# Optimization experiments

Measured on AMD Instinct MI355X. Metric: run time of the kernel, lower is better.

Reference implementation:

```python
import jax, jax.numpy as jnp
import numpy as np

BN_EPS = 1e-5
DIST_EPS = 1e-8


def setup_inputs() -> dict:
    key = jax.random.key(0)
    ks = jax.random.split(key, 10)
    B, Ni, Mi = 4, 16384, 4096
    C1, C2 = 64, 64
    Cin = C1 + C2  # 128, mlp=[128,128,128]
    inp = {
        "unknown": jax.random.normal(ks[0], (B * Ni, 3), dtype=jnp.float32),
        "unknown_batch_cnt": np.full(B, Ni, dtype=np.int64),
        "known": jax.random.normal(ks[1], (B * Mi, 3), dtype=jnp.float32),
        "known_batch_cnt": np.full(B, Mi, dtype=np.int64),
        "unknown_feats": jax.random.normal(ks[2], (B * Ni, C1), dtype=jnp.float32),
        "known_feats": jax.random.normal(ks[3], (B * Mi, C2), dtype=jnp.float32),
        "W1": jax.random.normal(ks[4], (128, Cin), dtype=jnp.float32) * 0.05,
        "g1": jnp.ones((128,), dtype=jnp.float32),
        "b1": jnp.zeros((128,), dtype=jnp.float32),
        "W2": jax.random.normal(ks[5], (128, 128), dtype=jnp.float32) * 0.05,
        "g2": jnp.ones((128,), dtype=jnp.float32),
        "b2": jnp.zeros((128,), dtype=jnp.float32),
    }
    return inp


def _three_nn(u, k):
    # u: (B,Ni,3), k: (B,Mi,3) -> dist (B,Ni,3), idx (B,Ni,3) within each batch
    d2 = (jnp.sum(u * u, -1)[:, :, None] + jnp.sum(k * k, -1)[:, None, :]
          - 2.0 * jnp.einsum("bnd,bmd->bnm", u, k))  # (B,Ni,Mi)
    neg_d2, idx = jax.lax.top_k(-d2, 3)
    dist = jnp.sqrt(jnp.maximum(-neg_d2, 0.0))
    return dist, idx


def _bn_relu(y, g, b):
    # BatchNorm2d over the point dim (training-mode batch stats), then ReLU
    mu = jnp.mean(y, axis=0)
    var = jnp.mean((y - mu) ** 2, axis=0)
    return jax.nn.relu((y - mu) * jax.lax.rsqrt(var + BN_EPS) * g + b)


def reference(unknown, unknown_batch_cnt, known, known_batch_cnt,
              unknown_feats, known_feats, W1, g1, b1, W2, g2, b2):
    ucnt = np.asarray(unknown_batch_cnt)
    kcnt = np.asarray(known_batch_cnt)
    B = ucnt.shape[0]
    Ni, Mi = int(ucnt[0]), int(kcnt[0])  # equal-count ragged batches
    C2 = known_feats.shape[1]

    u = unknown.reshape(B, Ni, 3)
    k = known.reshape(B, Mi, 3)
    dist, idx = _three_nn(u, k)

    dist_recip = 1.0 / (dist + DIST_EPS)
    weight = dist_recip / jnp.sum(dist_recip, axis=-1, keepdims=True)  # (B,Ni,3)

    kf = known_feats.reshape(B, Mi, C2)
    gathered = kf[jnp.arange(B)[:, None, None], idx]  # (B,Ni,3,C2)
    interp = jnp.sum(weight[..., None] * gathered, axis=2).reshape(B * Ni, C2)

    x = jnp.concatenate([interp, unknown_feats], axis=1)  # (N, C2+C1)
    x = _bn_relu(x @ W1.T, g1, b1)
    x = _bn_relu(x @ W2.T, g2, b2)
    return x
```

## Files before the change

### kernel.cpp

```cpp
#include <hip/hip_runtime.h>
#include <hip/hip_bf16.h>

#define GRID  32
#define NCELL (GRID * GRID * GRID)
#define H     0.3125f
#define INVH  3.2f
#define OFF   5.0f
#define SUBW  8
#define XPAD  136
#define NREP  16

using f32x4  = __attribute__((ext_vector_type(4))) float;
using bf16x8 = __attribute__((ext_vector_type(8))) short;

static __device__ inline short f2bs(float f) {
  __hip_bfloat16 h = __float2bfloat16(f);
  return __builtin_bit_cast(short, h);
}
static __device__ inline float bs2f(short s) {
  return __bfloat162float(__builtin_bit_cast(__hip_bfloat16, s));
}
static __device__ inline int cellco(float x) {
  int c = (int)((x + OFF) * INVH);
  return min(GRID - 1, max(0, c));
}

#define INS3(B0, B1, B2, J0, J1, J2, dv, mv)           \
  {                                                    \
    bool q0 = dv < B0, q1 = dv < B1, q2 = dv < B2;     \
    float P0 = B0, P1 = B1; int Q0 = J0, Q1 = J1;      \
    B2 = q1 ? P1 : (q2 ? dv : B2);                     \
    J2 = q1 ? Q1 : (q2 ? mv : J2);                     \
    B1 = q0 ? P0 : (q1 ? dv : P1);                     \
    J1 = q0 ? Q0 : (q1 ? mv : Q1);                     \
    B0 = q0 ? dv : P0;                                 \
    J0 = q0 ? mv : Q0;                                 \
  }
#define INSF(dv, mv) INS3(b0, b1, b2, j0, j1, j2, dv, mv)

#define MERGE3(lo_mk, hi_mk)                                                        \
  for (int mk = lo_mk; mk <= hi_mk; mk <<= 1) {                                     \
    float ob0 = __shfl_xor(b0, mk), ob1 = __shfl_xor(b1, mk), ob2 = __shfl_xor(b2, mk); \
    int   oj0 = __shfl_xor(j0, mk), oj1 = __shfl_xor(j1, mk), oj2 = __shfl_xor(j2, mk); \
    INSF(ob0, oj0); INSF(ob1, oj1); INSF(ob2, oj2);                                 \
  }

__global__ __launch_bounds__(256) void zero_k(int4* __restrict__ dst, int n4) {
  int i = blockIdx.x * 256 + threadIdx.x;
  if (i < n4) dst[i] = int4{0, 0, 0, 0};
}

__global__ __launch_bounds__(256) void hist_k(
    const float* __restrict__ known, int Mtot, int Mi,
    const float* __restrict__ unknown, int Ntot,
    int* __restrict__ khist, int* __restrict__ qhist,
    int* __restrict__ kcell, int* __restrict__ qcell,
    const float* __restrict__ W1, const float* __restrict__ W2,
    __hip_bfloat16* __restrict__ Wb1, __hip_bfloat16* __restrict__ Wb2) {
  int i = blockIdx.x * 256 + threadIdx.x;
  if (i < 128 * 128) {
    Wb1[i] = __float2bfloat16(W1[i]);
    Wb2[i] = __float2bfloat16(W2[i]);
  }
  if (i < Mtot) {
    int b = i / Mi;
    float x = known[(size_t)i * 3], y = known[(size_t)i * 3 + 1], z = known[(size_t)i * 3 + 2];
    int c = b * NCELL + (cellco(z) * GRID + cellco(y)) * GRID + cellco(x);
    kcell[i] = c;
    atomicAdd(&khist[c], 1);
  }
  if (i < Ntot) {
    int Ni = Ntot / (Mtot / Mi);
    int b = i / Ni;
    float x = unknown[(size_t)i * 3], y = unknown[(size_t)i * 3 + 1], z = unknown[(size_t)i * 3 + 2];
    int c = b * NCELL + (cellco(z) * GRID + cellco(y)) * GRID + cellco(x);
    qcell[i] = c;
    atomicAdd(&qhist[c], 1);
  }
}

__global__ __launch_bounds__(256) void scan1_k(
    const int4* __restrict__ Hc4, int* __restrict__ bsum) {
  __shared__ int sh[256];
  int t = threadIdx.x;
  int4 h = Hc4[blockIdx.x * 256 + t];
  int s = h.x + h.y + h.z + h.w;
  sh[t] = s;
  __syncthreads();
  for (int d = 128; d > 0; d >>= 1) {
    if (t < d) sh[t] += sh[t + d];
    __syncthreads();
  }
  if (t == 0) bsum[blockIdx.x] = sh[0];
}

__global__ __launch_bounds__(256) void scan3_k(
    const int4* __restrict__ Hc4, const int* __restrict__ bsum, int nbk,
    int* __restrict__ kstart, int* __restrict__ kfill,
    int* __restrict__ qstart, int* __restrict__ qfill,
    int nc, int Mtot, int Ntot) {
  __shared__ int sh[256];
  __shared__ int sv[256], sc[256];
  int t = threadIdx.x;
  int v = (t < nbk) ? bsum[t] : 0;
  sv[t] = v; sc[t] = v;
  int g4 = blockIdx.x * 256 + t;
  int4 h = Hc4[g4];
  int s = h.x + h.y + h.z + h.w;
  sh[t] = s;
  __syncthreads();
  for (int d = 1; d < 256; d <<= 1) {
    int u1 = (t >= d) ? sc[t - d] : 0;
    int u2 = (t >= d) ? sh[t - d] : 0;
    __syncthreads();
    sc[t] += u1;
    sh[t] += u2;
    __syncthreads();
  }
  int blockbase = sc[blockIdx.x] - sv[blockIdx.x];
  int run = blockbase + sh[t] - s;
  int hv[4] = {h.x, h.y, h.z, h.w};
#pragma unroll
  for (int j = 0; j < 4; ++j) {
    int g = g4 * 4 + j;
    if (g < nc) { kstart[g] = run; kfill[g] = run; }
    else        { int q = g - nc; qstart[q] = run - Mtot; qfill[q] = run - Mtot; }
    run += hv[j];
  }
  if (blockIdx.x == 0 && t == 0) { kstart[nc] = Mtot; qstart[nc] = Ntot; }
}

__global__ __launch_bounds__(256) void scatter_k(
    const float* __restrict__ known, int Mtot, int Mi,
    const float* __restrict__ unknown, int Ntot,
    const int* __restrict__ kcell, const int* __restrict__ qcell,
    int* __restrict__ kfill, int* __restrict__ qfill,
    f32x4* __restrict__ k4s, int* __restrict__ korder,
    f32x4* __restrict__ u4s, int* __restrict__ qorder) {
  int i = blockIdx.x * 256 + threadIdx.x;
  if (i < Mtot) {
    int slot = atomicAdd(&kfill[kcell[i]], 1);
    float x = known[(size_t)i * 3], y = known[(size_t)i * 3 + 1], z = known[(size_t)i * 3 + 2];
    f32x4 v;
    v[0] = -2.f * x; v[1] = -2.f * y; v[2] = -2.f * z;
    v[3] = x * x + y * y + z * z;
    k4s[slot] = v;
    korder[slot] = i - (i / Mi) * Mi;
  }
  if (i < Ntot) {
    int slot = atomicAdd(&qfill[qcell[i]], 1);
    float x = unknown[(size_t)i * 3], y = unknown[(size_t)i * 3 + 1], z = unknown[(size_t)i * 3 + 2];
    f32x4 v;
    v[0] = x; v[1] = y; v[2] = z;
    v[3] = __fmaf_rn(x, x, __fmaf_rn(y, y, z * z));
    u4s[slot] = v;
    qorder[slot] = i;
  }
}

static __device__ __forceinline__ void scan_box_strided(
    int R, int sub, int stride, int cx, int cy, int cz, int cellbase,
    const int* __restrict__ cstart, const f32x4* __restrict__ k4s,
    const int* __restrict__ korder,
    float ux, float uy, float uz,
    float& b0, float& b1, float& b2, int& j0, int& j1, int& j2) {
  int zlo = max(cz - R, 0), zhi = min(cz + R, GRID - 1);
  int ylo = max(cy - R, 0), yhi = min(cy + R, GRID - 1);
  int xlo = max(cx - R, 0), xhi = min(cx + R, GRID - 1);
  int ny = yhi - ylo + 1;
  int nrows = (zhi - zlo + 1) * ny;
  for (int rid = sub; rid < nrows; rid += stride) {
    int zz = rid / ny;
    int y  = ylo + (rid - zz * ny);
    int row = cellbase + ((zlo + zz) * GRID + y) * GRID;
    int s = cstart[row + xlo];
    int e = cstart[row + xhi + 1];
    for (int i = s; i < e; ++i) {
      f32x4 k = k4s[i];
      float d = __fmaf_rn(ux, k[0], __fmaf_rn(uy, k[1], __fmaf_rn(uz, k[2], k[3])));
      int m = korder[i];
      INSF(d, m);
    }
  }
}

static __device__ __forceinline__ void write_result(
    float* __restrict__ w, int* __restrict__ idx, int p, float uu,
    float b0, float b1, float b2, int j0, int j1, int j2) {
  float d0 = sqrtf(fmaxf(b0 + uu, 0.f));
  float d1 = sqrtf(fmaxf(b1 + uu, 0.f));
  float d2 = sqrtf(fmaxf(b2 + uu, 0.f));
  float r0 = 1.f / (d0 + 1e-8f);
  float r1 = 1.f / (d1 + 1e-8f);
  float r2 = 1.f / (d2 + 1e-8f);
  float rs = 1.f / (r0 + r1 + r2);
  size_t o = (size_t)p * 3;
  w[o] = r0 * rs; w[o + 1] = r1 * rs; w[o + 2] = r2 * rs;
  idx[o] = j0; idx[o + 1] = j1; idx[o + 2] = j2;
}

__global__ __launch_bounds__(256) void knn_grid_k(
    const f32x4* __restrict__ u4s, const int* __restrict__ qorder,
    const int* __restrict__ cstart, const f32x4* __restrict__ k4s,
    const int* __restrict__ korder, int Ni,
    float* __restrict__ w, int* __restrict__ idx) {
  int nwc = gridDim.x * 4;
  int gw  = blockIdx.x * 4 + (threadIdx.x >> 6);
  int wchunk = (gw * 997) & (nwc - 1);
  int lane = threadIdx.x & 63;
  int s   = wchunk * 8 + (lane / SUBW);
  int sub = threadIdx.x & (SUBW - 1);
  f32x4 u4 = u4s[s];
  int p = qorder[s];
  int b = p / Ni;
  float ux = u4[0], uy = u4[1], uz = u4[2], uu = u4[3];
  int cx = cellco(ux), cy = cellco(uy), cz = cellco(uz);
  int cellbase = b * NCELL;
  int xlo = max(cx - 1, 0), xhi = min(cx + 1, GRID - 1);

  float fx = (ux + OFF) * INVH - cx;
  float fy = (uy + OFF) * INVH - cy;
  float fz = (uz + OFF) * INVH - cz;
  float mf = fminf(fminf(fminf(fx, 1.f - fx), fminf(fy, 1.f - fy)),
                   fminf(fz, 1.f - fz));
  float cov = H * (1.f + fmaxf(mf, 0.f));
  float covsq = cov * cov;

  int cs[9], ce[9];
#pragma unroll
  for (int q = 0; q < 9; ++q) {
    int z = cz + (q / 3) - 1;
    int y = cy + (q % 3) - 1;
    bool valid = ((unsigned)z < GRID) && ((unsigned)y < GRID);
    int row = cellbase + (z * GRID + y) * GRID;
    int a0 = valid ? row + xlo : cellbase;
    int a1 = valid ? row + xhi + 1 : cellbase;
    cs[q] = cstart[a0];
    ce[q] = cstart[a1];
  }

  float b0 = 3e38f, b1 = 3e38f, b2 = 3e38f;
  int   j0 = 0,     j1 = 0,     j2 = 0;
  float e0 = 3e38f, e1 = 3e38f, e2 = 3e38f;
  int   f0 = 0,     f1 = 0,     f2 = 0;
#pragma unroll
  for (int q = 0; q < 9; ++q) {
    int i = cs[q] + sub;
    int e = ce[q];
    for (; i + SUBW < e; i += 2 * SUBW) {
      f32x4 kA = k4s[i];
      f32x4 kB = k4s[i + SUBW];
      int mA = korder[i];
      int mB = korder[i + SUBW];
      float dA = __fmaf_rn(ux, kA[0], __fmaf_rn(uy, kA[1], __fmaf_rn(uz, kA[2], kA[3])));
      float dB = __fmaf_rn(ux, kB[0], __fmaf_rn(uy, kB[1], __fmaf_rn(uz, kB[2], kB[3])));
      INS3(b0, b1, b2, j0, j1, j2, dA, mA);
      INS3(e0, e1, e2, f0, f1, f2, dB, mB);
    }
    if (i < e) {
      f32x4 kA = k4s[i];
      int mA = korder[i];
      float dA = __fmaf_rn(ux, kA[0], __fmaf_rn(uy, kA[1], __fmaf_rn(uz, kA[2], kA[3])));
      INS3(b0, b1, b2, j0, j1, j2, dA, mA);
    }
  }
  INSF(e0, f0); INSF(e1, f1); INSF(e2, f2);
  MERGE3(1, SUBW / 2);

  float d3sq = b2 + uu;
  bool ok = d3sq <= covsq;

  if (ok && sub == 0)
    write_result(w, idx, p, uu, b0, b1, b2, j0, j1, j2);

  unsigned long long mask = __ballot(!ok && sub == 0);
  while (mask) {
    int leader = __ffsll((long long)mask) - 1;
    mask &= mask - 1;
    float qux = __shfl(ux, leader);
    float quy = __shfl(uy, leader);
    float quz = __shfl(uz, leader);
    float quu = __shfl(uu, leader);
    float dd  = __shfl(d3sq, leader);
    int   qp  = __shfl(p, leader);
    int qb = qp / Ni;
    int qcx = cellco(qux), qcy = cellco(quy), qcz = cellco(quz);
    int qcb = qb * NCELL;
    int Rc = 1;
    bool done = false;
    float B0, B1, B2; int J0, J1, J2;
    while (!done) {
      if (dd < 1e30f) {
        Rc = max((int)ceilf(sqrtf(fmaxf(dd, 0.f)) * INVH), Rc + 1);
      } else {
        Rc = Rc * 2;
      }
      Rc = min(Rc, GRID);
      {
        float b0 = 3e38f, b1 = 3e38f, b2 = 3e38f;
        int   j0 = 0,     j1 = 0,     j2 = 0;
        scan_box_strided(Rc, lane, 64, qcx, qcy, qcz, qcb, cstart, k4s, korder,
                         qux, quy, quz, b0, b1, b2, j0, j1, j2);
        MERGE3(1, 32);
        B0 = b0; B1 = b1; B2 = b2; J0 = j0; J1 = j1; J2 = j2;
      }
      dd = B2 + quu;
      float cv = (float)Rc * H;
      done = (dd <= cv * cv) || (Rc >= GRID);
    }
    if (lane == 0)
      write_result(w, idx, qp, quu, B0, B1, B2, J0, J1, J2);
  }
}

template <bool F32OUT>
static __device__ __forceinline__ void gemm_half(
    const short* xs, const short* Ws, int row0,
    float* yf, __hip_bfloat16* yb, float* ls, float* lq) {
  int t = threadIdx.x;
  int lane = t & 63;
  int wv = t >> 6;
  int r = lane & 15, g = lane >> 4;
  int tile = wv >> 1, half = wv & 1;
  int trow = tile * 16;

  bf16x8 a[4];
#pragma unroll
  for (int q = 0; q < 4; ++q)
    a[q] = *reinterpret_cast<const bf16x8*>(&xs[(trow + r) * XPAD + g * 8 + q * 32]);

  int orow = row0 + trow + g * 4;
#pragma unroll
  for (int ct = 0; ct < 4; ++ct) {
    int ocol = half * 64 + ct * 16 + r;
    f32x4 acc = {0.f, 0.f, 0.f, 0.f};
    size_t bbase = (size_t)ocol * 128 + g * 8;
#pragma unroll
    for (int q = 0; q < 4; ++q) {
      bf16x8 bfr = *reinterpret_cast<const bf16x8*>(Ws + bbase + q * 32);
      acc = __builtin_amdgcn_mfma_f32_16x16x32_bf16(a[q], bfr, acc, 0, 0, 0);
    }
    if (F32OUT) {
#pragma unroll
      for (int i = 0; i < 4; ++i)
        yf[(size_t)(orow + i) * 128 + ocol] = acc[i];
    } else {
#pragma unroll
      for (int i = 0; i < 4; ++i)
        yb[(size_t)(orow + i) * 128 + ocol] = __float2bfloat16(acc[i]);
    }
    float s  = acc[0] + acc[1] + acc[2] + acc[3];
    float q2 = acc[0] * acc[0] + acc[1] * acc[1] + acc[2] * acc[2] + acc[3] * acc[3];
    s  += __shfl_xor(s, 16);  s  += __shfl_xor(s, 32);
    q2 += __shfl_xor(q2, 16); q2 += __shfl_xor(q2, 32);
    if (g == 0) {
      atomicAdd(&ls[ocol], s);
      atomicAdd(&lq[ocol], q2);
    }
  }
}

__global__ __launch_bounds__(256) void gemm1_fused_k(
    const float* __restrict__ kf, const float* __restrict__ uf,
    const float* __restrict__ wgt, const int* __restrict__ idx,
    const __hip_bfloat16* __restrict__ Wb, __hip_bfloat16* __restrict__ Yb,
    float* __restrict__ stats, int Ni, int Mi) {
  __shared__ short xs[32 * XPAD];
  __shared__ float ls[128], lq[128];
  int t = threadIdx.x;
  if (t < 128) { ls[t] = 0.f; lq[t] = 0.f; }
  int row0 = blockIdx.x * 32;

  int rr = t >> 3, c0 = (t & 7) * 16;
  int p = row0 + rr;
  short tmp[16];
  if (c0 < 64) {
    size_t o = (size_t)p * 3;
    float w0 = wgt[o], w1 = wgt[o + 1], w2 = wgt[o + 2];
    int i0 = idx[o], i1 = idx[o + 1], i2 = idx[o + 2];
    int b = p / Ni;
    const float* kfb = kf + (size_t)b * Mi * 64 + c0;
    const f32x4* r0p = reinterpret_cast<const f32x4*>(kfb + (size_t)i0 * 64);
    const f32x4* r1p = reinterpret_cast<const f32x4*>(kfb + (size_t)i1 * 64);
    const f32x4* r2p = reinterpret_cast<const f32x4*>(kfb + (size_t)i2 * 64);
#pragma unroll
    for (int j = 0; j < 4; ++j) {
      f32x4 av = r0p[j], bv = r1p[j], cv = r2p[j];
#pragma unroll
      for (int e = 0; e < 4; ++e)
        tmp[j * 4 + e] = f2bs(w0 * av[e] + w1 * bv[e] + w2 * cv[e]);
    }
  } else {
    const f32x4* ufp = reinterpret_cast<const f32x4*>(uf + (size_t)p * 64 + (c0 - 64));
#pragma unroll
    for (int j = 0; j < 4; ++j) {
      f32x4 av = ufp[j];
#pragma unroll
      for (int e = 0; e < 4; ++e)
        tmp[j * 4 + e] = f2bs(av[e]);
    }
  }
  *reinterpret_cast<bf16x8*>(&xs[rr * XPAD + c0])     = *reinterpret_cast<bf16x8*>(&tmp[0]);
  *reinterpret_cast<bf16x8*>(&xs[rr * XPAD + c0 + 8]) = *reinterpret_cast<bf16x8*>(&tmp[8]);
  __syncthreads();

  gemm_half<false>(xs, reinterpret_cast<const short*>(Wb), row0, nullptr, Yb, ls, lq);

  __syncthreads();
  if (t < 128) {
    int rep = blockIdx.x & (NREP - 1);
    atomicAdd(&stats[rep * 256 + t], ls[t]);
    atomicAdd(&stats[rep * 256 + 128 + t], lq[t]);
  }
}

__global__ __launch_bounds__(256) void gemm2_bn_k(
    const __hip_bfloat16* __restrict__ Y1, const float* __restrict__ stats,
    const float* __restrict__ g1, const float* __restrict__ b1v, float invN,
    const __hip_bfloat16* __restrict__ Wb, __hip_bfloat16* __restrict__ Yb2,
    float* __restrict__ stats2) {
  __shared__ short xs[32 * XPAD];
  __shared__ float ls[128], lq[128];
  __shared__ float ABs[256];
  int t = threadIdx.x;
  if (t < 128) {
    float s = 0.f, q = 0.f;
#pragma unroll
    for (int rpl = 0; rpl < NREP; ++rpl) {
      s += stats[rpl * 256 + t];
      q += stats[rpl * 256 + 128 + t];
    }
    float mu  = s * invN;
    float var = q * invN - mu * mu;
    float A = rsqrtf(var + 1e-5f) * g1[t];
    ABs[t] = A;
    ABs[128 + t] = b1v[t] - mu * A;
    ls[t] = 0.f; lq[t] = 0.f;
  }
  __syncthreads();
  int row0 = blockIdx.x * 32;

  int rr = t >> 3, c0 = (t & 7) * 16;
  int p = row0 + rr;
  const short* Ys = reinterpret_cast<const short*>(Y1);
  bf16x8 v0 = *reinterpret_cast<const bf16x8*>(Ys + (size_t)p * 128 + c0);
  bf16x8 v1 = *reinterpret_cast<const bf16x8*>(Ys + (size_t)p * 128 + c0 + 8);
  short tmp[16];
#pragma unroll
  for (int j = 0; j < 8; ++j)
    tmp[j] = f2bs(fmaxf(bs2f(v0[j]) * ABs[c0 + j] + ABs[128 + c0 + j], 0.f));
#pragma unroll
  for (int j = 0; j < 8; ++j)
    tmp[8 + j] = f2bs(fmaxf(bs2f(v1[j]) * ABs[c0 + 8 + j] + ABs[128 + c0 + 8 + j], 0.f));
  *reinterpret_cast<bf16x8*>(&xs[rr * XPAD + c0])     = *reinterpret_cast<bf16x8*>(&tmp[0]);
  *reinterpret_cast<bf16x8*>(&xs[rr * XPAD + c0 + 8]) = *reinterpret_cast<bf16x8*>(&tmp[8]);
  __syncthreads();

  gemm_half<false>(xs, reinterpret_cast<const short*>(Wb), row0, nullptr, Yb2, ls, lq);

  __syncthreads();
  if (t < 128) {
    int rep = blockIdx.x & (NREP - 1);
    atomicAdd(&stats2[rep * 256 + t], ls[t]);
    atomicAdd(&stats2[rep * 256 + 128 + t], lq[t]);
  }
}

__global__ __launch_bounds__(256) void bnrelu_out_k(
    const __hip_bfloat16* __restrict__ Y, const float* __restrict__ stats2,
    const float* __restrict__ g2, const float* __restrict__ b2v, float invN,
    float* __restrict__ Out, long n8) {
  __shared__ float ABs[256];
  int t = threadIdx.x;
  if (t < 128) {
    float s = 0.f, q = 0.f;
#pragma unroll
    for (int rpl = 0; rpl < NREP; ++rpl) {
      s += stats2[rpl * 256 + t];
      q += stats2[rpl * 256 + 128 + t];
    }
    float mu  = s * invN;
    float var = q * invN - mu * mu;
    float A = rsqrtf(var + 1e-5f) * g2[t];
    ABs[t] = A;
    ABs[128 + t] = b2v[t] - mu * A;
  }
  __syncthreads();
  long i = (long)blockIdx.x * 256 + t;
  long stride = (long)gridDim.x * 256;
  const bf16x8* Y8 = reinterpret_cast<const bf16x8*>(Y);
  for (; i < n8; i += stride) {
    bf16x8 y = Y8[i];
    int c0 = (int)((i * 8) & 127);
    f32x4 o0, o1;
#pragma unroll
    for (int j = 0; j < 4; ++j)
      o0[j] = fmaxf(bs2f(y[j]) * ABs[c0 + j] + ABs[128 + c0 + j], 0.f);
#pragma unroll
    for (int j = 0; j < 4; ++j)
      o1[j] = fmaxf(bs2f(y[4 + j]) * ABs[c0 + 4 + j] + ABs[128 + c0 + 4 + j], 0.f);
    reinterpret_cast<f32x4*>(Out)[i * 2]     = o0;
    reinterpret_cast<f32x4*>(Out)[i * 2 + 1] = o1;
  }
}

extern "C" void kernel_launch(void* const* d_in, const int* in_sizes, int n_in,
                              void* d_out, int out_size, void* d_ws, size_t ws_size,
                              hipStream_t stream) {
  const float* unknown = (const float*)d_in[0];
  const float* known   = (const float*)d_in[2];
  const float* uf      = (const float*)d_in[4];
  const float* kf      = (const float*)d_in[5];
  const float* W1      = (const float*)d_in[6];
  const float* g1      = (const float*)d_in[7];
  const float* b1      = (const float*)d_in[8];
  const float* W2      = (const float*)d_in[9];
  const float* g2      = (const float*)d_in[10];
  const float* b2      = (const float*)d_in[11];

  int B    = in_sizes[1];
  int Ntot = in_sizes[0] / 3;
  int Mtot = in_sizes[2] / 3;
  int Ni = Ntot / B, Mi = Mtot / B;
  int nc = B * NCELL;
  int n2 = 2 * nc;

  char* ws = (char*)d_ws;
  size_t off = 0;
  auto alloc = [&](size_t bytes) {
    void* p = ws + off;
    off += (bytes + 255) & ~(size_t)255;
    return p;
  };
  float* stats  = (float*)alloc(2 * NREP * 256 * 4);
  int*   khist  = (int*)alloc((size_t)n2 * 4);
  int*   qhist  = khist + nc;
  size_t zero_bytes = (size_t)((char*)(khist + n2) - (char*)stats);
  int*   kstart = (int*)alloc((size_t)(nc + 1) * 4);
  int*   qstart = (int*)alloc((size_t)(nc + 1) * 4);
  int*   kfill  = (int*)alloc((size_t)nc * 4);
  int*   qfill  = (int*)alloc((size_t)nc * 4);
  int*   kcell  = (int*)alloc((size_t)Mtot * 4);
  int*   qcell  = (int*)alloc((size_t)Ntot * 4);
  int*   korder = (int*)alloc((size_t)Mtot * 4);
  int*   qorder = (int*)alloc((size_t)Ntot * 4);
  int*   bsum   = (int*)alloc((size_t)(n2 / 1024) * 4);
  f32x4* k4s    = (f32x4*)alloc((size_t)Mtot * 16);
  f32x4* u4s    = (f32x4*)alloc((size_t)Ntot * 16);
  float* wgt    = (float*)alloc((size_t)Ntot * 3 * 4);
  int*   idx    = (int*)alloc((size_t)Ntot * 3 * 4);
  __hip_bfloat16* y1b = (__hip_bfloat16*)alloc((size_t)Ntot * 128 * 2);
  __hip_bfloat16* y2b = (__hip_bfloat16*)alloc((size_t)Ntot * 128 * 2);
  __hip_bfloat16* Wb1 = (__hip_bfloat16*)alloc(128 * 128 * 2);
  __hip_bfloat16* Wb2 = (__hip_bfloat16*)alloc(128 * 128 * 2);

  float* y2 = (float*)d_out;
  long n8 = (long)Ntot * 128 / 8;
  float invN = 1.0f / (float)Ntot;
  int nb = n2 / 1024;
  float* stats2 = stats + NREP * 256;
  int zn4 = (int)(zero_bytes / 16);

  zero_k<<<(zn4 + 255) / 256, 256, 0, stream>>>((int4*)stats, zn4);
  hist_k<<<(Ntot + 255) / 256, 256, 0, stream>>>(known, Mtot, Mi, unknown, Ntot,
                                                 khist, qhist, kcell, qcell, W1, W2, Wb1, Wb2);
  scan1_k<<<nb, 256, 0, stream>>>((const int4*)khist, bsum);
  scan3_k<<<nb, 256, 0, stream>>>((const int4*)khist, bsum, nb, kstart, kfill,
                                  qstart, qfill, nc, Mtot, Ntot);
  scatter_k<<<(Ntot + 255) / 256, 256, 0, stream>>>(known, Mtot, Mi, unknown, Ntot,
                                                    kcell, qcell, kfill, qfill, k4s, korder, u4s, qorder);
  knn_grid_k<<<Ntot / 32, 256, 0, stream>>>(u4s, qorder, kstart, k4s, korder, Ni, wgt, idx);
  gemm1_fused_k<<<Ntot / 32, 256, 0, stream>>>(kf, uf, wgt, idx, Wb1, y1b, stats, Ni, Mi);
  gemm2_bn_k<<<Ntot / 32, 256, 0, stream>>>(y1b, stats, g1, b1, invN, Wb2, y2b, stats2);
  bnrelu_out_k<<<2048, 256, 0, stream>>>(y2b, stats2, g2, b2, invN, y2, n8);
}
```

Baseline: 168.0 us.

## Defer failed KNN queries to a separate retry kernel via atomic worklist

Queries whose first 3x3x3-cell search cannot guarantee the three nearest neighbours are no longer retried inside the main KNN kernel's wave loop. They are appended through an atomic counter to a compacted list, and a second kernel processes that list with one wavefront per query. This is meant to stop a few slow queries from holding whole wavefronts of the main kernel and to spread the retry work evenly. It costs an extra kernel launch, global atomics, and reloading each retried query's data.

Measured after the change: 144.1 us, median of 2. -14.2%, faster.

```diff
diff --git a/kernel.cpp b/kernel.cpp
--- a/kernel.cpp
+++ b/kernel.cpp
@@ -203,12 +203,12 @@
     const f32x4* __restrict__ u4s, const int* __restrict__ qorder,
     const int* __restrict__ cstart, const f32x4* __restrict__ k4s,
     const int* __restrict__ korder, int Ni,
-    float* __restrict__ w, int* __restrict__ idx) {
+    float* __restrict__ w, int* __restrict__ idx,
+    int* __restrict__ rcnt, int* __restrict__ rlist, float* __restrict__ rd3) {
   int nwc = gridDim.x * 4;
   int gw  = blockIdx.x * 4 + (threadIdx.x >> 6);
   int wchunk = (gw * 997) & (nwc - 1);
-  int lane = threadIdx.x & 63;
-  int s   = wchunk * 8 + (lane / SUBW);
+  int s   = wchunk * 8 + ((threadIdx.x & 63) / SUBW);
   int sub = threadIdx.x & (SUBW - 1);
   f32x4 u4 = u4s[s];
   int p = qorder[s];
@@ -270,46 +270,58 @@
   float d3sq = b2 + uu;
   bool ok = d3sq <= covsq;
 
-  if (ok && sub == 0)
-    write_result(w, idx, p, uu, b0, b1, b2, j0, j1, j2);
-
-  unsigned long long mask = __ballot(!ok && sub == 0);
-  while (mask) {
-    int leader = __ffsll((long long)mask) - 1;
-    mask &= mask - 1;
-    float qux = __shfl(ux, leader);
-    float quy = __shfl(uy, leader);
-    float quz = __shfl(uz, leader);
-    float quu = __shfl(uu, leader);
-    float dd  = __shfl(d3sq, leader);
-    int   qp  = __shfl(p, leader);
-    int qb = qp / Ni;
-    int qcx = cellco(qux), qcy = cellco(quy), qcz = cellco(quz);
-    int qcb = qb * NCELL;
+  if (sub == 0) {
+    if (ok) {
+      write_result(w, idx, p, uu, b0, b1, b2, j0, j1, j2);
+    } else {
+      int t = atomicAdd(rcnt, 1);
+      rlist[t] = s;
+      rd3[t] = d3sq;
+    }
+  }
+}
+
+__global__ __launch_bounds__(256) void knn_retry_k(
+    const f32x4* __restrict__ u4s, const int* __restrict__ qorder,
+    const int* __restrict__ rlist, const float* __restrict__ rd3,
+    const int* __restrict__ rcnt,
+    const int* __restrict__ cstart, const f32x4* __restrict__ k4s,
+    const int* __restrict__ korder, int Ni,
+    float* __restrict__ w, int* __restrict__ idx) {
+  int lane = threadIdx.x & 63;
+  int wv   = blockIdx.x * 4 + (threadIdx.x >> 6);
+  int nw   = gridDim.x * 4;
+  int cnt  = rcnt[0];
+  for (int q = wv; q < cnt; q += nw) {
+    int sq = rlist[q];
+    f32x4 u4 = u4s[sq];
+    int p = qorder[sq];
+    int b = p / Ni;
+    float ux = u4[0], uy = u4[1], uz = u4[2], uu = u4[3];
+    int cx = cellco(ux), cy = cellco(uy), cz = cellco(uz);
+    int cellbase = b * NCELL;
+
+    float d3sq = rd3[q];
     int Rc = 1;
-    bool done = false;
-    float B0, B1, B2; int J0, J1, J2;
-    while (!done) {
-      if (dd < 1e30f) {
-        Rc = max((int)ceilf(sqrtf(fmaxf(dd, 0.f)) * INVH), Rc + 1);
+    float b0, b1, b2; int j0, j1, j2;
+    bool ok = false;
+    while (!ok) {
+      if (d3sq < 1e30f) {
+        Rc = max((int)ceilf(sqrtf(fmaxf(d3sq, 0.f)) * INVH), Rc + 1);
       } else {
         Rc = Rc * 2;
       }
       Rc = min(Rc, GRID);
-      {
-        float b0 = 3e38f, b1 = 3e38f, b2 = 3e38f;
-        int   j0 = 0,     j1 = 0,     j2 = 0;
-        scan_box_strided(Rc, lane, 64, qcx, qcy, qcz, qcb, cstart, k4s, korder,
-                         qux, quy, quz, b0, b1, b2, j0, j1, j2);
-        MERGE3(1, 32);
-        B0 = b0; B1 = b1; B2 = b2; J0 = j0; J1 = j1; J2 = j2;
-      }
-      dd = B2 + quu;
-      float cv = (float)Rc * H;
-      done = (dd <= cv * cv) || (Rc >= GRID);
+      b0 = b1 = b2 = 3e38f; j0 = j1 = j2 = 0;
+      scan_box_strided(Rc, lane, 64, cx, cy, cz, cellbase, cstart, k4s, korder,
+                       ux, uy, uz, b0, b1, b2, j0, j1, j2);
+      MERGE3(1, 32);
+      d3sq = b2 + uu;
+      float cov = (float)Rc * H;
+      ok = (d3sq <= cov * cov) || (Rc >= GRID);
     }
     if (lane == 0)
-      write_result(w, idx, qp, quu, B0, B1, B2, J0, J1, J2);
+      write_result(w, idx, p, uu, b0, b1, b2, j0, j1, j2);
   }
 }
 
@@ -533,6 +545,7 @@
     return p;
   };
   float* stats  = (float*)alloc(2 * NREP * 256 * 4);
+  int*   rcnt   = (int*)alloc(4);
   int*   khist  = (int*)alloc((size_t)n2 * 4);
   int*   qhist  = khist + nc;
   size_t zero_bytes = (size_t)((char*)(khist + n2) - (char*)stats);
@@ -545,6 +558,8 @@
   int*   korder = (int*)alloc((size_t)Mtot * 4);
   int*   qorder = (int*)alloc((size_t)Ntot * 4);
   int*   bsum   = (int*)alloc((size_t)(n2 / 1024) * 4);
+  int*   rlist  = (int*)alloc((size_t)Ntot * 4);
+  float* rd3    = (float*)alloc((size_t)Ntot * 4);
   f32x4* k4s    = (f32x4*)alloc((size_t)Mtot * 16);
   f32x4* u4s    = (f32x4*)alloc((size_t)Ntot * 16);
   float* wgt    = (float*)alloc((size_t)Ntot * 3 * 4);
@@ -569,7 +584,10 @@
                                   qstart, qfill, nc, Mtot, Ntot);
   scatter_k<<<(Ntot + 255) / 256, 256, 0, stream>>>(known, Mtot, Mi, unknown, Ntot,
                                                     kcell, qcell, kfill, qfill, k4s, korder, u4s, qorder);
-  knn_grid_k<<<Ntot / 32, 256, 0, stream>>>(u4s, qorder, kstart, k4s, korder, Ni, wgt, idx);
+  knn_grid_k<<<Ntot / 32, 256, 0, stream>>>(u4s, qorder, kstart, k4s, korder, Ni,
+                                            wgt, idx, rcnt, rlist, rd3);
+  knn_retry_k<<<1024, 256, 0, stream>>>(u4s, qorder, rlist, rd3, rcnt,
+                                        kstart, k4s, korder, Ni, wgt, idx);
   gemm1_fused_k<<<Ntot / 32, 256, 0, stream>>>(kf, uf, wgt, idx, Wb1, y1b, stats, Ni, Mi);
   gemm2_bn_k<<<Ntot / 32, 256, 0, stream>>>(y1b, stats, g1, b1, invN, Wb2, y2b, stats2);
   bnrelu_out_k<<<2048, 256, 0, stream>>>(y2b, stats2, g2, b2, invN, y2, n8);
```
